# Kernel optimization log

Hardware: AMD Instinct MI355X
Metric: run time of the kernel (lower is better)

## Reference

```python
import jax, jax.numpy as jnp
import numpy as np

B, S, D, H, MLP_D = 2, 2048, 512, 8, 128
DH = D // H  # 64
EPS = 1e-5


def setup_inputs() -> dict:
    key = jax.random.key(0)
    ks = jax.random.split(key, 8)
    return {
        "z": jax.random.normal(ks[0], (B, S, D), dtype=jnp.float32),
        "head_w": jax.random.normal(ks[1], (H, D, 3 * DH), dtype=jnp.float32),
        "w_o": jax.random.normal(ks[2], (H * DH, D), dtype=jnp.float32),
        "ln_w": jnp.ones((D,), dtype=jnp.float32),
        "ln_b": jnp.zeros((D,), dtype=jnp.float32),
        "w1": jax.random.normal(ks[3], (D, MLP_D), dtype=jnp.float32) * (1.0 / np.sqrt(D)),
        "b1": jnp.zeros((MLP_D,), dtype=jnp.float32),
        "w2": jax.random.normal(ks[4], (MLP_D, D), dtype=jnp.float32) * (1.0 / np.sqrt(MLP_D)),
        "b2": jnp.zeros((D,), dtype=jnp.float32),
    }


def _layernorm(x, w, b):
    mu = jnp.mean(x, axis=-1, keepdims=True)
    var = jnp.var(x, axis=-1, keepdims=True)
    return (x - mu) * jax.lax.rsqrt(var + EPS) * w + b


def reference(z, head_w, w_o, ln_w, ln_b, w1, b1, w2, b2):
    # --- MSA block: z = MSA(LN(z)) + z ---
    x = _layernorm(z, ln_w, ln_b)                       # [B,S,D]
    qkv = jnp.einsum("bsd,hde->bhse", x, head_w)        # [B,H,S,3*DH]
    q, k, v = qkv[..., :DH], qkv[..., DH:2 * DH], qkv[..., 2 * DH:]
    scores = jnp.einsum("bhsd,bhtd->bhst", q, k) / jnp.sqrt(jnp.float32(DH))
    p = jax.nn.softmax(scores, axis=-1)                 # [B,H,S,S]
    o = jnp.einsum("bhst,bhtd->bhsd", p, v)             # [B,H,S,DH]
    # concat heads along last dim (head order matches torch.cat), then project
    o = jnp.transpose(o, (0, 2, 1, 3)).reshape(B, S, H * DH)
    z = o @ w_o + z
    # --- MLP block: z = GELU(Linear2(Linear1(LN(z)))) + z (GELU last, per Sequential) ---
    y = _layernorm(z, ln_w, ln_b)
    y = (y @ w1 + b1) @ w2 + b2
    z = jax.nn.gelu(y, approximate=False) + z
    return z
```

## Files before the change

### kernel.cpp

```cpp
#include <hip/hip_runtime.h>
#include <hip/hip_bf16.h>

typedef unsigned short u16;
typedef unsigned int u32;
typedef __attribute__((ext_vector_type(8))) short short8;
typedef __attribute__((ext_vector_type(8))) __bf16 bf16x8;
typedef __attribute__((ext_vector_type(4))) float f32x4;

#define DEV static __device__ __forceinline__

DEV float bf2f(u16 u) { unsigned v = ((unsigned)u) << 16; float f; __builtin_memcpy(&f, &v, 4); return f; }
DEV u16 f2bf(float f) {
  unsigned u; __builtin_memcpy(&u, &f, 4);
  unsigned lsb = (u >> 16) & 1;
  u += 0x7fffu + lsb;
  return (u16)(u >> 16);
}
DEV float exp2fast(float x) { return __builtin_amdgcn_exp2f(x); }
DEV f32x4 mfma16(short8 a, short8 b, f32x4 c) {
  return __builtin_amdgcn_mfma_f32_16x16x32_bf16(
      __builtin_bit_cast(bf16x8, a), __builtin_bit_cast(bf16x8, b), c, 0, 0, 0);
}
DEV short8 ld8(const u16* p) { return *(const short8*)p; }

__global__ void prep_all(const float* __restrict__ hw, const float* __restrict__ wo,
                         const float* __restrict__ w1, const float* __restrict__ w2,
                         u16* __restrict__ wqh, u16* __restrict__ wql,
                         u16* __restrict__ woT, u16* __restrict__ w1T, u16* __restrict__ w2T) {
  int idx = blockIdx.x * 256 + threadIdx.x;
  if (idx < 786432) {
    int e = idx % 192;
    int d = (idx / 192) % 512;
    int h = idx / (192 * 512);
    float v = hw[idx];
    int n = (e < 64) ? (h * 64 + e) : (e < 128) ? (512 + h * 64 + e - 64) : (1024 + h * 64 + e - 128);
    size_t oi = (size_t)n * 512 + d;
    u16 hh = f2bf(v);
    wqh[oi] = hh;
    if (e < 128) wql[oi] = f2bf(v - bf2f(hh));
  } else if (idx < 786432 + 262144) {
    int i = idx - 786432;
    int n = i % 512, k = i / 512;
    woT[(size_t)n * 512 + k] = f2bf(wo[i]);
  } else if (idx < 786432 + 262144 + 65536) {
    int i = idx - (786432 + 262144);
    int n = i % 128, k = i / 128;
    w1T[(size_t)n * 512 + k] = f2bf(w1[i]);
  } else if (idx < 786432 + 262144 + 131072) {
    int i = idx - (786432 + 262144 + 65536);
    int n = i % 512, k = i / 512;
    w2T[(size_t)n * 128 + k] = f2bf(w2[i]);
  }
}

__global__ __launch_bounds__(256) void ln_kernel(const float* __restrict__ in,
                                                 const float* __restrict__ w,
                                                 const float* __restrict__ bb,
                                                 u16* __restrict__ hi, u16* __restrict__ lo) {
  const int wv = threadIdx.x >> 6, lane = threadIdx.x & 63;
  const int row = blockIdx.x * 4 + wv;
  const float4* r = (const float4*)(in + (size_t)row * 512);
  float4 a0 = r[lane * 2], a1 = r[lane * 2 + 1];
  float s = a0.x + a0.y + a0.z + a0.w + a1.x + a1.y + a1.z + a1.w;
  float ss = a0.x * a0.x + a0.y * a0.y + a0.z * a0.z + a0.w * a0.w +
             a1.x * a1.x + a1.y * a1.y + a1.z * a1.z + a1.w * a1.w;
#pragma unroll
  for (int m = 1; m < 64; m <<= 1) { s += __shfl_xor(s, m); ss += __shfl_xor(ss, m); }
  float mu = s * (1.f / 512.f);
  float var = ss * (1.f / 512.f) - mu * mu;
  float rstd = rsqrtf(var + 1e-5f);
  const float4* wp = (const float4*)w + lane * 2;
  const float4* bp = (const float4*)bb + lane * 2;
  float4 w0 = wp[0], w1v = wp[1], b0 = bp[0], b1v = bp[1];
  float xv[8] = {a0.x, a0.y, a0.z, a0.w, a1.x, a1.y, a1.z, a1.w};
  float wv8[8] = {w0.x, w0.y, w0.z, w0.w, w1v.x, w1v.y, w1v.z, w1v.w};
  float bv8[8] = {b0.x, b0.y, b0.z, b0.w, b1v.x, b1v.y, b1v.z, b1v.w};
  short8 oh, ol;
#pragma unroll
  for (int i = 0; i < 8; i++) {
    float v = (xv[i] - mu) * rstd * wv8[i] + bv8[i];
    u16 hh = f2bf(v);
    oh[i] = (short)hh;
    ol[i] = (short)f2bf(v - bf2f(hh));
  }
  *(short8*)(hi + (size_t)row * 512 + lane * 8) = oh;
  *(short8*)(lo + (size_t)row * 512 + lane * 8) = ol;
}

__global__ __launch_bounds__(256) void gemm_qkv(const u16* __restrict__ Ah, const u16* __restrict__ Alo,
                                                const u16* __restrict__ Bh, const u16* __restrict__ Blo,
                                                u16* __restrict__ qkh, u16* __restrict__ qkl,
                                                u16* __restrict__ vT) {
  __shared__ __align__(16) u16 As[128][40], Asl[128][40], Bs[64][40], Bsl[64][40];
  const int tid = threadIdx.x, lane = tid & 63, wv = tid >> 6;
  const int wm = wv >> 1, wn = wv & 1, g = lane >> 4, r16 = lane & 15;
  const int bm = blockIdx.x * 128, bn = blockIdx.y * 64;
  const bool split = blockIdx.y < 16;
  short8 sA[2], sAl[2], sB, sBl;
  auto ldtile = [&](int kt) {
#pragma unroll
    for (int c = 0; c < 2; c++) {
      int ch = c * 256 + tid;
      sA[c] = ld8(Ah + (size_t)(bm + (ch >> 2)) * 512 + kt + (ch & 3) * 8);
      if (split) sAl[c] = ld8(Alo + (size_t)(bm + (ch >> 2)) * 512 + kt + (ch & 3) * 8);
    }
    sB = ld8(Bh + (size_t)(bn + (tid >> 2)) * 512 + kt + (tid & 3) * 8);
    if (split) sBl = ld8(Blo + (size_t)(bn + (tid >> 2)) * 512 + kt + (tid & 3) * 8);
  };
  f32x4 acc[4][2] = {};
  ldtile(0);
  for (int kt = 0; kt < 512; kt += 32) {
    __syncthreads();
#pragma unroll
    for (int c = 0; c < 2; c++) {
      int ch = c * 256 + tid;
      *(short8*)&As[ch >> 2][(ch & 3) * 8] = sA[c];
      if (split) *(short8*)&Asl[ch >> 2][(ch & 3) * 8] = sAl[c];
    }
    *(short8*)&Bs[tid >> 2][(tid & 3) * 8] = sB;
    if (split) *(short8*)&Bsl[tid >> 2][(tid & 3) * 8] = sBl;
    __syncthreads();
    if (kt + 32 < 512) ldtile(kt + 32);
    short8 af[4], bf_[2], afl[4], bfl[2];
#pragma unroll
    for (int mi = 0; mi < 4; mi++) af[mi] = *(const short8*)&As[wm * 64 + mi * 16 + r16][g * 8];
#pragma unroll
    for (int ni = 0; ni < 2; ni++) bf_[ni] = *(const short8*)&Bs[wn * 32 + ni * 16 + r16][g * 8];
    if (split) {
#pragma unroll
      for (int mi = 0; mi < 4; mi++) afl[mi] = *(const short8*)&Asl[wm * 64 + mi * 16 + r16][g * 8];
#pragma unroll
      for (int ni = 0; ni < 2; ni++) bfl[ni] = *(const short8*)&Bsl[wn * 32 + ni * 16 + r16][g * 8];
    }
#pragma unroll
    for (int mi = 0; mi < 4; mi++)
#pragma unroll
      for (int ni = 0; ni < 2; ni++) {
        acc[mi][ni] = mfma16(af[mi], bf_[ni], acc[mi][ni]);
        if (split) {
          acc[mi][ni] = mfma16(af[mi], bfl[ni], acc[mi][ni]);
          acc[mi][ni] = mfma16(afl[mi], bf_[ni], acc[mi][ni]);
        }
      }
  }
#pragma unroll
  for (int mi = 0; mi < 4; mi++)
#pragma unroll
    for (int ni = 0; ni < 2; ni++) {
      int col = bn + wn * 32 + ni * 16 + r16;
      int row0 = bm + wm * 64 + mi * 16 + g * 4;
      if (split) {
#pragma unroll
        for (int j = 0; j < 4; j++) {
          size_t oi = (size_t)(row0 + j) * 1024 + col;
          float v = acc[mi][ni][j];
          u16 hh = f2bf(v);
          qkh[oi] = hh;
          qkl[oi] = f2bf(v - bf2f(hh));
        }
      } else {
        int vcol = col - 1024;
        ushort4 pk;
        pk.x = f2bf(acc[mi][ni][0]);
        pk.y = f2bf(acc[mi][ni][1]);
        pk.z = f2bf(acc[mi][ni][2]);
        pk.w = f2bf(acc[mi][ni][3]);
        *(ushort4*)(vT + (size_t)vcol * 4096 + row0) = pk;
      }
    }
}

template <int MF, int NF, int EPI>
__global__ __launch_bounds__(256) void gemm_g(const u16* __restrict__ A, const u16* __restrict__ BT,
                                              const float* __restrict__ res, const float* __restrict__ bias,
                                              u16* __restrict__ outb, float* __restrict__ outf,
                                              int N, int K) {
  constexpr int BM = 32 * MF, BN = 32 * NF;
  constexpr int CA = (BM * 4 + 255) / 256, CB = (BN * 4 + 255) / 256;
  __shared__ __align__(16) u16 As[BM][40], Bs[BN][40];
  const int tid = threadIdx.x, lane = tid & 63, wv = tid >> 6;
  const int wm = wv >> 1, wn = wv & 1, g = lane >> 4, r16 = lane & 15;
  const int bm = blockIdx.x * BM, bn = blockIdx.y * BN;
  short8 sA[CA], sB[CB];
  auto ldtile = [&](int kt) {
#pragma unroll
    for (int c = 0; c < CA; c++) {
      int ch = c * 256 + tid;
      if (ch < BM * 4) sA[c] = ld8(A + (size_t)(bm + (ch >> 2)) * K + kt + (ch & 3) * 8);
    }
#pragma unroll
    for (int c = 0; c < CB; c++) {
      int ch = c * 256 + tid;
      if (ch < BN * 4) sB[c] = ld8(BT + (size_t)(bn + (ch >> 2)) * K + kt + (ch & 3) * 8);
    }
  };
  f32x4 acc[MF][NF] = {};
  ldtile(0);
  for (int kt = 0; kt < K; kt += 32) {
    __syncthreads();
#pragma unroll
    for (int c = 0; c < CA; c++) {
      int ch = c * 256 + tid;
      if (ch < BM * 4) *(short8*)&As[ch >> 2][(ch & 3) * 8] = sA[c];
    }
#pragma unroll
    for (int c = 0; c < CB; c++) {
      int ch = c * 256 + tid;
      if (ch < BN * 4) *(short8*)&Bs[ch >> 2][(ch & 3) * 8] = sB[c];
    }
    __syncthreads();
    if (kt + 32 < K) ldtile(kt + 32);
    short8 af[MF], bf_[NF];
#pragma unroll
    for (int mi = 0; mi < MF; mi++) af[mi] = *(const short8*)&As[wm * 16 * MF + mi * 16 + r16][g * 8];
#pragma unroll
    for (int ni = 0; ni < NF; ni++) bf_[ni] = *(const short8*)&Bs[wn * 16 * NF + ni * 16 + r16][g * 8];
#pragma unroll
    for (int mi = 0; mi < MF; mi++)
#pragma unroll
      for (int ni = 0; ni < NF; ni++) acc[mi][ni] = mfma16(af[mi], bf_[ni], acc[mi][ni]);
  }
#pragma unroll
  for (int mi = 0; mi < MF; mi++)
#pragma unroll
    for (int ni = 0; ni < NF; ni++) {
      int col = bn + wn * 16 * NF + ni * 16 + r16;
      int row0 = bm + wm * 16 * MF + mi * 16 + g * 4;
#pragma unroll
      for (int j = 0; j < 4; j++) {
        size_t oi = (size_t)(row0 + j) * N + col;
        float v = acc[mi][ni][j];
        if (EPI == 1) {
          outf[oi] = v + res[oi];
        } else if (EPI == 2) {
          outb[oi] = f2bf(v + bias[col]);
        } else {
          float u = v + bias[col];
          float gl = 0.5f * u * (1.0f + erff(u * 0.70710678118f));
          outf[oi] = gl + res[oi];
        }
      }
    }
}

__global__ __launch_bounds__(128, 2) void attn_kernel(const u16* __restrict__ qkh,
                                                      const u16* __restrict__ qkl,
                                                      const u16* __restrict__ vT,
                                                      u16* __restrict__ o) {
  constexpr int SK = 72, SV = 136, SP = 136;
  __shared__ __align__(16) u16 Kh[128 * SK], Kl[128 * SK], Vt[64 * SV];
  __shared__ __align__(16) u16 Pl[2][32 * SP];
  const int tid = threadIdx.x, lane = tid & 63, w = tid >> 6;
  const int g = lane >> 4, r16 = lane & 15;
  const int qb = blockIdx.x * 64;
  const int b = blockIdx.y >> 3, h = blockIdx.y & 7;
  const size_t bbase = (size_t)b * 2048 * 1024;
  const u16* Qh = qkh + bbase + h * 64;
  const u16* Ql = qkl + bbase + h * 64;
  const u16* KgH = qkh + bbase + 512 + h * 64;
  const u16* KgL = qkl + bbase + 512 + h * 64;
  const u16* Vtg = vT + (size_t)h * 64 * 4096 + (size_t)b * 2048;

  short8 qh[2][2], qlo[2][2];
#pragma unroll
  for (int t = 0; t < 2; t++) {
    int qrow = qb + w * 32 + t * 16 + r16;
#pragma unroll
    for (int ks = 0; ks < 2; ks++) {
      qh[t][ks] = ld8(Qh + (size_t)qrow * 1024 + ks * 32 + g * 8);
      qlo[t][ks] = ld8(Ql + (size_t)qrow * 1024 + ks * 32 + g * 8);
    }
  }

  f32x4 oacc[2][4] = {};
  float m_r[2] = {-3e38f, -3e38f}, l_r[2] = {0.f, 0.f};

  short8 kA[8], kB[8], vS[8];
  auto ldkv = [&](int kt) {
#pragma unroll
    for (int c = 0; c < 8; c++) {
      int kr = c * 16 + (tid >> 3), kc = (tid & 7) * 8;
      kA[c] = ld8(KgH + (size_t)(kt + kr) * 1024 + kc);
      kB[c] = ld8(KgL + (size_t)(kt + kr) * 1024 + kc);
    }
#pragma unroll
    for (int c = 0; c < 8; c++) {
      int vd = c * 8 + (tid >> 4), vc = (tid & 15) * 8;
      vS[c] = ld8(Vtg + (size_t)vd * 4096 + kt + vc);
    }
  };
  ldkv(0);

  for (int kt = 0; kt < 2048; kt += 128) {
    __syncthreads();
#pragma unroll
    for (int c = 0; c < 8; c++) {
      int kr = c * 16 + (tid >> 3), kc = (tid & 7) * 8;
      *(short8*)&Kh[kr * SK + kc] = kA[c];
      *(short8*)&Kl[kr * SK + kc] = kB[c];
    }
#pragma unroll
    for (int c = 0; c < 8; c++) {
      int vd = c * 8 + (tid >> 4), vc = (tid & 15) * 8;
      *(short8*)&Vt[vd * SV + vc] = vS[c];
    }
    __syncthreads();
    if (kt + 128 < 2048) ldkv(kt + 128);
    f32x4 s[2][8];
#pragma unroll
    for (int t = 0; t < 2; t++)
#pragma unroll
      for (int f = 0; f < 8; f++) s[t][f] = f32x4{0.f, 0.f, 0.f, 0.f};
#pragma unroll
    for (int f = 0; f < 8; f++) {
      int krow = f * 16 + r16;
#pragma unroll
      for (int ks = 0; ks < 2; ks++) {
        short8 bh = *(const short8*)&Kh[krow * SK + ks * 32 + g * 8];
        short8 bl = *(const short8*)&Kl[krow * SK + ks * 32 + g * 8];
#pragma unroll
        for (int t = 0; t < 2; t++) {
          s[t][f] = mfma16(bh, qh[t][ks], s[t][f]);
          s[t][f] = mfma16(bl, qh[t][ks], s[t][f]);
          s[t][f] = mfma16(bh, qlo[t][ks], s[t][f]);
        }
      }
    }
    constexpr float SCL2 = 0.125f * 1.44269504f;
    float scl[2];
#pragma unroll
    for (int t = 0; t < 2; t++) {
      float a[8][4];
      float vm = -3e38f;
#pragma unroll
      for (int f = 0; f < 8; f++)
#pragma unroll
        for (int r = 0; r < 4; r++) {
          a[f][r] = s[t][f][r] * SCL2;
          vm = fmaxf(vm, a[f][r]);
        }
      vm = fmaxf(vm, __shfl_xor(vm, 16));
      vm = fmaxf(vm, __shfl_xor(vm, 32));
      float mn = fmaxf(m_r[t], vm);
      scl[t] = exp2fast(m_r[t] - mn);
      m_r[t] = mn;
      float rs = 0.f;
#pragma unroll
      for (int f = 0; f < 8; f++) {
        float e0 = exp2fast(a[f][0] - mn), e1 = exp2fast(a[f][1] - mn);
        float e2 = exp2fast(a[f][2] - mn), e3 = exp2fast(a[f][3] - mn);
        rs += (e0 + e1) + (e2 + e3);
        u32 u0, u1, u2, u3;
        __builtin_memcpy(&u0, &e0, 4);
        __builtin_memcpy(&u1, &e1, 4);
        __builtin_memcpy(&u2, &e2, 4);
        __builtin_memcpy(&u3, &e3, 4);
        uint2 pk;
        pk.x = (u0 >> 16) | (u1 & 0xFFFF0000u);
        pk.y = (u2 >> 16) | (u3 & 0xFFFF0000u);
        *(uint2*)&Pl[w][(t * 16 + r16) * SP + f * 16 + g * 4] = pk;
      }
      rs += __shfl_xor(rs, 16);
      rs += __shfl_xor(rs, 32);
      l_r[t] = l_r[t] * scl[t] + rs;
    }
#pragma unroll
    for (int t = 0; t < 2; t++)
#pragma unroll
      for (int j = 0; j < 4; j++) {
        float sj = __shfl(scl[t], (g << 4) + (g << 2) + j);
#pragma unroll
        for (int dt = 0; dt < 4; dt++) oacc[t][dt][j] *= sj;
      }
#pragma unroll
    for (int ks = 0; ks < 4; ks++) {
      short8 pa0 = *(const short8*)&Pl[w][(0 * 16 + r16) * SP + ks * 32 + g * 8];
      short8 pa1 = *(const short8*)&Pl[w][(1 * 16 + r16) * SP + ks * 32 + g * 8];
#pragma unroll
      for (int dt = 0; dt < 4; dt++) {
        short8 vb = *(const short8*)&Vt[(dt * 16 + r16) * SV + ks * 32 + g * 8];
        oacc[0][dt] = mfma16(pa0, vb, oacc[0][dt]);
        oacc[1][dt] = mfma16(pa1, vb, oacc[1][dt]);
      }
    }
  }
#pragma unroll
  for (int t = 0; t < 2; t++)
#pragma unroll
    for (int j = 0; j < 4; j++) {
      float lj = __shfl(l_r[t], (g << 4) + (g << 2) + j);
      float il = 1.f / lj;
      int row = b * 2048 + qb + w * 32 + t * 16 + g * 4 + j;
#pragma unroll
      for (int dt = 0; dt < 4; dt++) {
        int col = h * 64 + dt * 16 + r16;
        o[(size_t)row * 512 + col] = f2bf(oacc[t][dt][j] * il);
      }
    }
}

extern "C" void kernel_launch(void* const* d_in, const int* in_sizes, int n_in,
                              void* d_out, int out_size, void* d_ws, size_t ws_size,
                              hipStream_t stream) {
  const float* z = (const float*)d_in[0];
  const float* head_w = (const float*)d_in[1];
  const float* w_o = (const float*)d_in[2];
  const float* ln_w = (const float*)d_in[3];
  const float* ln_b = (const float*)d_in[4];
  const float* w1 = (const float*)d_in[5];
  const float* b1 = (const float*)d_in[6];
  const float* w2 = (const float*)d_in[7];
  const float* b2 = (const float*)d_in[8];
  float* out = (float*)d_out;

  size_t off = 0;
  auto alc = [&](size_t n) {
    void* p = (char*)d_ws + off;
    off += (n + 255) & ~(size_t)255;
    return p;
  };
  u16* x_hi = (u16*)alc((size_t)4096 * 512 * 2);
  u16* x_lo = (u16*)alc((size_t)4096 * 512 * 2);
  u16* wqh = (u16*)alc((size_t)1536 * 512 * 2);
  u16* wql = (u16*)alc((size_t)1536 * 512 * 2);
  u16* woT = (u16*)alc((size_t)512 * 512 * 2);
  u16* w1T = (u16*)alc((size_t)128 * 512 * 2);
  u16* w2T = (u16*)alc((size_t)512 * 128 * 2);
  u16* qkh = (u16*)alc((size_t)4096 * 1024 * 2);
  u16* qkl = (u16*)alc((size_t)4096 * 1024 * 2);
  u16* vT = (u16*)alc((size_t)512 * 4096 * 2);
  u16* ob = (u16*)alc((size_t)4096 * 512 * 2);
  float* z2 = (float*)alc((size_t)4096 * 512 * 4);
  u16* tb = (u16*)alc((size_t)4096 * 128 * 2);

  prep_all<<<4608, 256, 0, stream>>>(head_w, w_o, w1, w2, wqh, wql, woT, w1T, w2T);

  ln_kernel<<<1024, 256, 0, stream>>>(z, ln_w, ln_b, x_hi, x_lo);

  gemm_qkv<<<dim3(32, 24), 256, 0, stream>>>(x_hi, x_lo, wqh, wql, qkh, qkl, vT);

  attn_kernel<<<dim3(32, 16), 128, 0, stream>>>(qkh, qkl, vT, ob);

  gemm_g<2, 2, 1><<<dim3(64, 8), 256, 0, stream>>>(ob, woT, z, nullptr, nullptr, z2, 512, 512);

  ln_kernel<<<1024, 256, 0, stream>>>(z2, ln_w, ln_b, x_hi, x_lo);

  gemm_g<1, 2, 2><<<dim3(128, 2), 256, 0, stream>>>(x_hi, w1T, nullptr, b1, tb, nullptr, 128, 512);

  gemm_g<2, 2, 3><<<dim3(64, 8), 256, 0, stream>>>(tb, w2T, z2, b2, nullptr, out, 512, 128);
}
```

Baseline: 139.3 us.

## Split attention KV sequence across two wave pairs and merge softmax partials

```diff
diff --git a/kernel.cpp b/kernel.cpp
--- a/kernel.cpp
+++ b/kernel.cpp
@@ -243,15 +243,18 @@
     }
 }
 
-__global__ __launch_bounds__(128, 2) void attn_kernel(const u16* __restrict__ qkh,
-                                                      const u16* __restrict__ qkl,
-                                                      const u16* __restrict__ vT,
-                                                      u16* __restrict__ o) {
-  constexpr int SK = 72, SV = 136, SP = 136;
-  __shared__ __align__(16) u16 Kh[128 * SK], Kl[128 * SK], Vt[64 * SV];
-  __shared__ __align__(16) u16 Pl[2][32 * SP];
+__global__ __launch_bounds__(256) void attn_kernel(const u16* __restrict__ qkh,
+                                                   const u16* __restrict__ qkl,
+                                                   const u16* __restrict__ vT,
+                                                   u16* __restrict__ o) {
+  __shared__ __align__(16) u16 smem[36864];
+  u16* Kh = smem;
+  u16* Kl = smem + 9216;
+  u16* Vt = smem + 18432;
   const int tid = threadIdx.x, lane = tid & 63, w = tid >> 6;
+  const int qg = w & 1, half = w >> 1;
   const int g = lane >> 4, r16 = lane & 15;
+  u16* Pw = smem + 27648 + w * 2304;
   const int qb = blockIdx.x * 64;
   const int b = blockIdx.y >> 3, h = blockIdx.y & 7;
   const size_t bbase = (size_t)b * 2048 * 1024;
@@ -264,7 +267,7 @@
   short8 qh[2][2], qlo[2][2];
 #pragma unroll
   for (int t = 0; t < 2; t++) {
-    int qrow = qb + w * 32 + t * 16 + r16;
+    int qrow = qb + qg * 32 + t * 16 + r16;
 #pragma unroll
     for (int ks = 0; ks < 2; ks++) {
       qh[t][ks] = ld8(Qh + (size_t)qrow * 1024 + ks * 32 + g * 8);
@@ -275,49 +278,54 @@
   f32x4 oacc[2][4] = {};
   float m_r[2] = {-3e38f, -3e38f}, l_r[2] = {0.f, 0.f};
 
-  short8 kA[8], kB[8], vS[8];
+  short8 kA[4], kB[4], vS[4];
   auto ldkv = [&](int kt) {
 #pragma unroll
-    for (int c = 0; c < 8; c++) {
-      int kr = c * 16 + (tid >> 3), kc = (tid & 7) * 8;
-      kA[c] = ld8(KgH + (size_t)(kt + kr) * 1024 + kc);
-      kB[c] = ld8(KgL + (size_t)(kt + kr) * 1024 + kc);
-    }
-#pragma unroll
-    for (int c = 0; c < 8; c++) {
-      int vd = c * 8 + (tid >> 4), vc = (tid & 15) * 8;
-      vS[c] = ld8(Vtg + (size_t)vd * 4096 + kt + vc);
+    for (int c = 0; c < 4; c++) {
+      int ch = c * 256 + tid;
+      int kr = ch >> 3, kc = (ch & 7) * 8;
+      int grow = kt + (kr & 63) + (kr >> 6) * 1024;
+      kA[c] = ld8(KgH + (size_t)grow * 1024 + kc);
+      kB[c] = ld8(KgL + (size_t)grow * 1024 + kc);
+    }
+#pragma unroll
+    for (int c = 0; c < 4; c++) {
+      int ch = c * 256 + tid;
+      int vr = ch >> 3, vc = (ch & 7) * 8;
+      vS[c] = ld8(Vtg + (size_t)(vr & 63) * 4096 + kt + (vr >> 6) * 1024 + vc);
     }
   };
   ldkv(0);
 
-  for (int kt = 0; kt < 2048; kt += 128) {
-    __syncthreads();
-#pragma unroll
-    for (int c = 0; c < 8; c++) {
-      int kr = c * 16 + (tid >> 3), kc = (tid & 7) * 8;
-      *(short8*)&Kh[kr * SK + kc] = kA[c];
-      *(short8*)&Kl[kr * SK + kc] = kB[c];
-    }
-#pragma unroll
-    for (int c = 0; c < 8; c++) {
-      int vd = c * 8 + (tid >> 4), vc = (tid & 15) * 8;
-      *(short8*)&Vt[vd * SV + vc] = vS[c];
-    }
-    __syncthreads();
-    if (kt + 128 < 2048) ldkv(kt + 128);
-    f32x4 s[2][8];
+  for (int kt = 0; kt < 1024; kt += 64) {
+    __syncthreads();
+#pragma unroll
+    for (int c = 0; c < 4; c++) {
+      int ch = c * 256 + tid;
+      int kr = ch >> 3, kc = (ch & 7) * 8;
+      *(short8*)&Kh[kr * 72 + kc] = kA[c];
+      *(short8*)&Kl[kr * 72 + kc] = kB[c];
+    }
+#pragma unroll
+    for (int c = 0; c < 4; c++) {
+      int ch = c * 256 + tid;
+      int vr = ch >> 3, vc = (ch & 7) * 8;
+      *(short8*)&Vt[vr * 72 + vc] = vS[c];
+    }
+    __syncthreads();
+    if (kt + 64 < 1024) ldkv(kt + 64);
+    f32x4 s[2][4];
 #pragma unroll
     for (int t = 0; t < 2; t++)
 #pragma unroll
-      for (int f = 0; f < 8; f++) s[t][f] = f32x4{0.f, 0.f, 0.f, 0.f};
-#pragma unroll
-    for (int f = 0; f < 8; f++) {
-      int krow = f * 16 + r16;
+      for (int f = 0; f < 4; f++) s[t][f] = f32x4{0.f, 0.f, 0.f, 0.f};
+#pragma unroll
+    for (int f = 0; f < 4; f++) {
+      int krow = half * 64 + f * 16 + r16;
 #pragma unroll
       for (int ks = 0; ks < 2; ks++) {
-        short8 bh = *(const short8*)&Kh[krow * SK + ks * 32 + g * 8];
-        short8 bl = *(const short8*)&Kl[krow * SK + ks * 32 + g * 8];
+        short8 bh = *(const short8*)&Kh[krow * 72 + ks * 32 + g * 8];
+        short8 bl = *(const short8*)&Kl[krow * 72 + ks * 32 + g * 8];
 #pragma unroll
         for (int t = 0; t < 2; t++) {
           s[t][f] = mfma16(bh, qh[t][ks], s[t][f]);
@@ -330,10 +338,10 @@
     float scl[2];
 #pragma unroll
     for (int t = 0; t < 2; t++) {
-      float a[8][4];
+      float a[4][4];
       float vm = -3e38f;
 #pragma unroll
-      for (int f = 0; f < 8; f++)
+      for (int f = 0; f < 4; f++)
 #pragma unroll
         for (int r = 0; r < 4; r++) {
           a[f][r] = s[t][f][r] * SCL2;
@@ -346,7 +354,7 @@
       m_r[t] = mn;
       float rs = 0.f;
 #pragma unroll
-      for (int f = 0; f < 8; f++) {
+      for (int f = 0; f < 4; f++) {
         float e0 = exp2fast(a[f][0] - mn), e1 = exp2fast(a[f][1] - mn);
         float e2 = exp2fast(a[f][2] - mn), e3 = exp2fast(a[f][3] - mn);
         rs += (e0 + e1) + (e2 + e3);
@@ -358,7 +366,7 @@
         uint2 pk;
         pk.x = (u0 >> 16) | (u1 & 0xFFFF0000u);
         pk.y = (u2 >> 16) | (u3 & 0xFFFF0000u);
-        *(uint2*)&Pl[w][(t * 16 + r16) * SP + f * 16 + g * 4] = pk;
+        *(uint2*)&Pw[(t * 16 + r16) * 72 + f * 16 + g * 4] = pk;
       }
       rs += __shfl_xor(rs, 16);
       rs += __shfl_xor(rs, 32);
@@ -373,30 +381,55 @@
         for (int dt = 0; dt < 4; dt++) oacc[t][dt][j] *= sj;
       }
 #pragma unroll
-    for (int ks = 0; ks < 4; ks++) {
-      short8 pa0 = *(const short8*)&Pl[w][(0 * 16 + r16) * SP + ks * 32 + g * 8];
-      short8 pa1 = *(const short8*)&Pl[w][(1 * 16 + r16) * SP + ks * 32 + g * 8];
+    for (int ks = 0; ks < 2; ks++) {
+      short8 pa0 = *(const short8*)&Pw[(0 * 16 + r16) * 72 + ks * 32 + g * 8];
+      short8 pa1 = *(const short8*)&Pw[(1 * 16 + r16) * 72 + ks * 32 + g * 8];
 #pragma unroll
       for (int dt = 0; dt < 4; dt++) {
-        short8 vb = *(const short8*)&Vt[(dt * 16 + r16) * SV + ks * 32 + g * 8];
+        short8 vb = *(const short8*)&Vt[(half * 64 + dt * 16 + r16) * 72 + ks * 32 + g * 8];
         oacc[0][dt] = mfma16(pa0, vb, oacc[0][dt]);
         oacc[1][dt] = mfma16(pa1, vb, oacc[1][dt]);
       }
     }
   }
-#pragma unroll
-  for (int t = 0; t < 2; t++)
-#pragma unroll
-    for (int j = 0; j < 4; j++) {
-      float lj = __shfl(l_r[t], (g << 4) + (g << 2) + j);
-      float il = 1.f / lj;
-      int row = b * 2048 + qb + w * 32 + t * 16 + g * 4 + j;
-#pragma unroll
-      for (int dt = 0; dt < 4; dt++) {
-        int col = h * 64 + dt * 16 + r16;
-        o[(size_t)row * 512 + col] = f2bf(oacc[t][dt][j] * il);
-      }
-    }
+  __syncthreads();
+  float* oex = (float*)smem;
+  float2* mlx = (float2*)(smem + 8192);
+  if (half == 1) {
+#pragma unroll
+    for (int t = 0; t < 2; t++) {
+#pragma unroll
+      for (int dt = 0; dt < 4; dt++)
+#pragma unroll
+        for (int j = 0; j < 4; j++)
+          oex[((qg * 2 + t) * 16 + g * 4 + j) * 64 + dt * 16 + r16] = oacc[t][dt][j];
+      if (g == 0) mlx[(qg * 2 + t) * 16 + r16] = make_float2(m_r[t], l_r[t]);
+    }
+  }
+  __syncthreads();
+  if (half == 0) {
+#pragma unroll
+    for (int t = 0; t < 2; t++)
+#pragma unroll
+      for (int j = 0; j < 4; j++) {
+        int rr = g * 4 + j;
+        float m0 = __shfl(m_r[t], (g << 4) + (g << 2) + j);
+        float l0 = __shfl(l_r[t], (g << 4) + (g << 2) + j);
+        float2 ml1 = mlx[(qg * 2 + t) * 16 + rr];
+        float mm = fmaxf(m0, ml1.x);
+        float c0 = exp2fast(m0 - mm), c1 = exp2fast(ml1.x - mm);
+        float inv = 1.f / (c0 * l0 + c1 * ml1.y);
+        c0 *= inv;
+        c1 *= inv;
+        int row = b * 2048 + qb + qg * 32 + t * 16 + rr;
+#pragma unroll
+        for (int dt = 0; dt < 4; dt++) {
+          float o1 = oex[((qg * 2 + t) * 16 + rr) * 64 + dt * 16 + r16];
+          int col = h * 64 + dt * 16 + r16;
+          o[(size_t)row * 512 + col] = f2bf(oacc[t][dt][j] * c0 + o1 * c1);
+        }
+      }
+  }
 }
 
 extern "C" void kernel_launch(void* const* d_in, const int* in_sizes, int n_in,
@@ -439,7 +472,7 @@
 
   gemm_qkv<<<dim3(32, 24), 256, 0, stream>>>(x_hi, x_lo, wqh, wql, qkh, qkl, vT);
 
-  attn_kernel<<<dim3(32, 16), 128, 0, stream>>>(qkh, qkl, vT, ob);
+  attn_kernel<<<dim3(32, 16), 256, 0, stream>>>(qkh, qkl, vT, ob);
 
   gemm_g<2, 2, 1><<<dim3(64, 8), 256, 0, stream>>>(ob, woT, z, nullptr, nullptr, z2, 512, 512);
 
```

Measured after the change: 132.3 us. 1.05x faster.
